# Kernel tuning notes

Measured on AMD Instinct MI355X. Metric: run time of the kernel, lower is better.

## Reference

```python
import jax, jax.numpy as jnp
import numpy as np

NU, NS, NV = 50000, 10000, 30000
D = 128
NUM_LAYERS = 2
EPS_US, EPS_UV, EPS_SV = 0.1, 0.1, 0.1
C_TEMP = 0.2
B = 2048


def _l2(x, eps=1e-12):
    n = jnp.sqrt(jnp.sum(x * x, axis=-1, keepdims=True))
    return x / jnp.maximum(n, eps)


def _spmm(row, col, val, x, n_out):
    # COO sparse @ dense: gather rows of x, scale, segment-reduce
    return jax.ops.segment_sum(val[:, None] * x[col], row, num_segments=n_out)


def _propagate(row, col, val, a, b, eps, key):
    feats = jnp.concatenate([a, b], axis=0)
    n = feats.shape[0]
    acc = feats  # layer-0 features are NOT normalized in the original
    for i in range(NUM_LAYERS):
        feats = _spmm(row, col, val, feats, n)
        noise = jax.random.uniform(jax.random.fold_in(key, i), feats.shape, feats.dtype)
        feats = feats + jnp.sign(feats) * _l2(noise) * eps
        acc = acc + _l2(feats)
    mean = acc / (NUM_LAYERS + 1)
    return mean[: a.shape[0]], mean[a.shape[0]:]


def _aggregate(row, col, val, x, n_out, eps, key):
    agg = _spmm(row, col, val, x, n_out)
    noise = jax.random.uniform(key, agg.shape, agg.dtype)
    return agg + jnp.sign(agg) * _l2(noise) * eps


def _mga(users_list, streamers_list, lin_w, lin_b):
    embs = [jnp.concatenate([u, s], axis=0) for u, s in zip(users_list, streamers_list)]
    query = jnp.stack(embs, axis=1)                      # (N, 3, D)
    key_e = jnp.broadcast_to(embs[0][:, None, :], query.shape)
    concat = jnp.concatenate([key_e, query], axis=2)     # (N, 3, 2D)
    logits = jnp.einsum('nkc,c->nk', concat, lin_w[0]) + lin_b[0]
    att = jax.nn.softmax(logits, axis=1)                 # (N, 3)
    out = jnp.einsum('nk,nkd->nd', att, query)
    return out[:NU], out[NU:]


def _c_loss(x):
    p = _l2(x[:, 0, :])
    pos = jnp.sum(p * p, axis=1) / C_TEMP
    ttl = jax.nn.logsumexp(p @ p.T / C_TEMP, axis=1)
    return -jnp.mean(pos - ttl)


def _forward(users_feature, streamers_feature, videos_feature, lin_w, lin_b,
             us_row, us_col, us_val, uv_row, uv_col, uv_val,
             sv_row, sv_col, sv_val,
             uv_agg_row, uv_agg_col, uv_agg_val,
             sv_agg_row, sv_agg_col, sv_agg_val, users, streamers):
    key = jax.random.key(42)
    k_us, k_uv, k_sv, k_auv, k_asv = jax.random.split(key, 5)
    US_u, US_s = _propagate(us_row, us_col, us_val, users_feature, streamers_feature, EPS_US, k_us)
    UV_u, UV_v = _propagate(uv_row, uv_col, uv_val, users_feature, videos_feature, EPS_UV, k_uv)
    UV_s = _aggregate(sv_agg_row, sv_agg_col, sv_agg_val, UV_v, NS, EPS_SV, k_asv)
    SV_s, SV_v = _propagate(sv_row, sv_col, sv_val, streamers_feature, videos_feature, EPS_SV, k_sv)
    SV_u = _aggregate(uv_agg_row, uv_agg_col, uv_agg_val, SV_v, NU, EPS_UV, k_auv)
    users_rep, streamers_rep = _mga([US_u, UV_u, SV_u], [US_s, UV_s, SV_s], lin_w, lin_b)
    s_emb = streamers_rep[streamers]                      # (B, K, D)
    u_emb = jnp.broadcast_to(users_rep[users], s_emb.shape)  # (B, K, D)
    pred = jnp.sum(u_emb * s_emb, axis=2)                 # (B, K)
    bpr = -jnp.mean(jax.nn.log_sigmoid(pred[:, :1] - pred[:, 1:]))
    c_loss = 0.5 * (_c_loss(u_emb) + _c_loss(s_emb))
    return bpr, c_loss


def setup_inputs() -> dict:
    rng = np.random.default_rng(0)

    def prop_graph(m, n, nnz):
        r = rng.integers(0, m, nnz)
        c = rng.integers(0, n, nnz)
        rows = np.concatenate([r, c + m])
        cols = np.concatenate([c + m, r])
        deg = np.bincount(rows, minlength=m + n).astype(np.float64)
        d = 1.0 / (np.sqrt(deg) + 1e-8)
        vals = (d[rows] * d[cols]).astype(np.float32)
        return rows.astype(np.int32), cols.astype(np.int32), vals, r, c

    def agg_graph(r, c, m):
        rowsum = np.bincount(r, minlength=m).astype(np.float64)
        vals = (1.0 / (rowsum + 1e-8))[r].astype(np.float32)
        return r.astype(np.int32), c.astype(np.int32), vals

    us_row, us_col, us_val, _, _ = prop_graph(NU, NS, 400000)
    uv_row, uv_col, uv_val, uv_r, uv_c = prop_graph(NU, NV, 600000)
    sv_row, sv_col, sv_val, sv_r, sv_c = prop_graph(NS, NV, 400000)
    uv_agg_row, uv_agg_col, uv_agg_val = agg_graph(uv_r, uv_c, NU)
    sv_agg_row, sv_agg_col, sv_agg_val = agg_graph(sv_r, sv_c, NS)

    key = jax.random.key(0)
    k1, k2, k3, k4, k6, k7 = jax.random.split(key, 6)
    xn = lambda k, m: jax.random.normal(k, (m, D), jnp.float32) * np.sqrt(2.0 / (m + D)).astype(np.float32)
    return {
        'users_feature': xn(k1, NU),
        'streamers_feature': xn(k2, NS),
        'videos_feature': xn(k3, NV),
        'lin_w': jax.random.uniform(k4, (1, 2 * D), jnp.float32, -1.0, 1.0) * np.sqrt(6.0 / (2 * D + 1)).astype(np.float32),
        'lin_b': jnp.zeros((1,), jnp.float32),
        'us_row': jnp.asarray(us_row), 'us_col': jnp.asarray(us_col), 'us_val': jnp.asarray(us_val),
        'uv_row': jnp.asarray(uv_row), 'uv_col': jnp.asarray(uv_col), 'uv_val': jnp.asarray(uv_val),
        'sv_row': jnp.asarray(sv_row), 'sv_col': jnp.asarray(sv_col), 'sv_val': jnp.asarray(sv_val),
        'uv_agg_row': jnp.asarray(uv_agg_row), 'uv_agg_col': jnp.asarray(uv_agg_col), 'uv_agg_val': jnp.asarray(uv_agg_val),
        'sv_agg_row': jnp.asarray(sv_agg_row), 'sv_agg_col': jnp.asarray(sv_agg_col), 'sv_agg_val': jnp.asarray(sv_agg_val),
        'users': jax.random.randint(k6, (B, 1), 0, NU, dtype=jnp.int32),
        'streamers': jax.random.randint(k7, (B, 2), 0, NS, dtype=jnp.int32),
    }


def reference(users_feature, streamers_feature, videos_feature, lin_w, lin_b,
              us_row, us_col, us_val, uv_row, uv_col, uv_val,
              sv_row, sv_col, sv_val,
              uv_agg_row, uv_agg_col, uv_agg_val,
              sv_agg_row, sv_agg_col, sv_agg_val, users, streamers):
    return _forward(users_feature, streamers_feature, videos_feature, lin_w, lin_b,
                    us_row, us_col, us_val, uv_row, uv_col, uv_val,
                    sv_row, sv_col, sv_val,
                    uv_agg_row, uv_agg_col, uv_agg_val,
                    sv_agg_row, sv_agg_col, sv_agg_val, users, streamers)
```

## Files before the change

### kernel.cpp

```cpp
#include <hip/hip_runtime.h>
#include <stdint.h>

#define D 128
constexpr int NUc = 50000, NSc = 10000, NVc = 30000, Bc = 2048;
constexpr int N_US = 60000, N_UV = 80000, N_SV = 40000, N_ALL = 90000;
constexpr int BW = 64;
constexpr int NBH = 1280;
constexpr int CHUNK = 4096;
constexpr int CAPE = 6144;

typedef _Float16 h2v __attribute__((ext_vector_type(2)));
typedef _Float16 h4v __attribute__((ext_vector_type(4)));

__host__ __device__ inline void threefry(uint32_t k0, uint32_t k1, uint32_t x0, uint32_t x1,
                                         uint32_t& o0, uint32_t& o1) {
  uint32_t ks2 = k0 ^ k1 ^ 0x1BD11BDAu;
  uint32_t v0 = x0 + k0, v1 = x1 + k1;
#define TFR(r) { v0 += v1; v1 = (v1 << (r)) | (v1 >> (32 - (r))); v1 ^= v0; }
  TFR(13) TFR(15) TFR(26) TFR(6)   v0 += k1;  v1 += ks2 + 1u;
  TFR(17) TFR(29) TFR(16) TFR(24)  v0 += ks2; v1 += k0 + 2u;
  TFR(13) TFR(15) TFR(26) TFR(6)   v0 += k0;  v1 += k1 + 3u;
  TFR(17) TFR(29) TFR(16) TFR(24)  v0 += k1;  v1 += ks2 + 4u;
  TFR(13) TFR(15) TFR(26) TFR(6)   v0 += ks2; v1 += k0 + 5u;
#undef TFR
  o0 = v0; o1 = v1;
}

__device__ __forceinline__ float unif01(uint32_t k0, uint32_t k1, uint32_t j) {
  uint32_t a, b;
  threefry(k0, k1, 0u, j, a, b);
  uint32_t bits = a ^ b;
  return __uint_as_float(0x3F800000u | (bits >> 9)) - 1.0f;
}

struct Bld {
  const int* rows[5]; const int* cols[5]; const float* vals[5];
  int* rp[5]; int* aux[5];
  int2* cv[5]; int2* ibuf[5];
  int* bhist;
  int eBase[6];
  int sBlkBase[6];
  int cBlkBase[6];
  int bktBase[6];
  int nPlus1[5];
};

__global__ void k_hist5(Bld b) {
  int gid = blockIdx.x * blockDim.x + threadIdx.x;
  if (gid >= b.eBase[5]) return;
  int g = 0;
  while (gid >= b.eBase[g + 1]) ++g;
  int e = gid - b.eBase[g];
  atomicAdd(&b.rp[g][b.rows[g][e] + 1], 1);
}

__global__ __launch_bounds__(1024) void k_scan1f(Bld b) {
  __shared__ int wsum[16];
  int blk = blockIdx.x;
  int g = 0;
  while (blk >= b.sBlkBase[g + 1]) ++g;
  int lb = blk - b.sBlkBase[g];
  int n = b.nPlus1[g];
  int* data = b.rp[g];
  int tid = threadIdx.x, lane = tid & 63, w = tid >> 6;
  int i = lb * 1024 + tid;
  int x = (i < n) ? data[i] : 0;
  for (int off = 1; off < 64; off <<= 1) {
    int t = __shfl_up(x, off, 64);
    if (lane >= off) x += t;
  }
  if (lane == 63) wsum[w] = x;
  __syncthreads();
  if (w == 0 && lane < 16) {
    int s = wsum[lane];
    for (int off = 1; off < 16; off <<= 1) {
      int t = __shfl_up(s, off, 64);
      if (lane >= off) s += t;
    }
    wsum[lane] = s;
  }
  __syncthreads();
  int woff = (w > 0) ? wsum[w - 1] : 0;
  if (i < n) data[i] = x + woff;
  if (tid == 1023) b.aux[g][lb] = x + woff;
}

__global__ void k_scan2f(Bld b) {
  int g = blockIdx.x;
  int nb = b.sBlkBase[g + 1] - b.sBlkBase[g];
  int* aux = b.aux[g];
  int lane = threadIdx.x;
  int carry = 0;
  for (int base = 0; base < nb; base += 64) {
    int i = base + lane;
    int v = (i < nb) ? aux[i] : 0;
    for (int off = 1; off < 64; off <<= 1) {
      int t = __shfl_up(v, off, 64);
      if (lane >= off) v += t;
    }
    if (i < nb) aux[i] = v + carry;
    carry += __shfl(v, 63, 64);
  }
}

__global__ __launch_bounds__(1024) void k_scan3f(Bld b) {
  int blk = blockIdx.x;
  int g = 0;
  while (blk >= b.sBlkBase[g + 1]) ++g;
  int lb = blk - b.sBlkBase[g];
  if (lb == 0) return;
  int i = lb * 1024 + threadIdx.x;
  if (i < b.nPlus1[g]) b.rp[g][i] += b.aux[g][lb - 1];
}

__global__ __launch_bounds__(256) void k_bhist(Bld b) {
  __shared__ int h[NBH];
  int blk = blockIdx.x;
  int g = 0;
  while (blk >= b.cBlkBase[g + 1]) ++g;
  int lblk = blk - b.cBlkBase[g];
  int nbkt = b.bktBase[g + 1] - b.bktBase[g];
  int tid = threadIdx.x;
  for (int i = tid; i < nbkt; i += 256) h[i] = 0;
  __syncthreads();
  int nnzg = b.eBase[g + 1] - b.eBase[g];
  int e0 = lblk * CHUNK;
  int eEnd = min(e0 + CHUNK, nnzg);
  for (int e = e0 + tid; e < eEnd; e += 256)
    atomicAdd(&h[b.rows[g][e] >> 6], 1);
  __syncthreads();
  int* outp = b.bhist + (size_t)blk * NBH;
  for (int i = tid; i < nbkt; i += 256) outp[i] = h[i];
}

__global__ void k_bscan(Bld b) {
  int gid = blockIdx.x * blockDim.x + threadIdx.x;
  int w = gid >> 6, lane = gid & 63;
  if (w >= b.bktBase[5]) return;
  int g = 0;
  while (w >= b.bktBase[g + 1]) ++g;
  int lb = w - b.bktBase[g];
  int carry = b.rp[g][lb * BW];
  int blk0 = b.cBlkBase[g], nblk = b.cBlkBase[g + 1] - blk0;
  for (int t = 0; t < nblk; t += 64) {
    int i = t + lane;
    int v = (i < nblk) ? b.bhist[(size_t)(blk0 + i) * NBH + lb] : 0;
    int x = v;
    for (int off = 1; off < 64; off <<= 1) {
      int tt = __shfl_up(x, off, 64);
      if (lane >= off) x += tt;
    }
    if (i < nblk) b.bhist[(size_t)(blk0 + i) * NBH + lb] = x - v + carry;
    carry += __shfl(x, 63, 64);
  }
}

__global__ __launch_bounds__(256) void k_bscat(Bld b) {
  __shared__ int cur[NBH];
  int blk = blockIdx.x;
  int g = 0;
  while (blk >= b.cBlkBase[g + 1]) ++g;
  int lblk = blk - b.cBlkBase[g];
  int nbkt = b.bktBase[g + 1] - b.bktBase[g];
  int tid = threadIdx.x;
  const int* bh = b.bhist + (size_t)blk * NBH;
  for (int i = tid; i < nbkt; i += 256) cur[i] = bh[i];
  __syncthreads();
  int nnzg = b.eBase[g + 1] - b.eBase[g];
  int e0 = lblk * CHUNK;
  int eEnd = min(e0 + CHUNK, nnzg);
  int2* ib = b.ibuf[g];
  for (int e = e0 + tid; e < eEnd; e += 256) {
    int row = b.rows[g][e];
    int pos = atomicAdd(&cur[row >> 6], 1);
    int packed = b.cols[g][e] | ((row & (BW - 1)) << 17);
    ib[pos] = make_int2(packed, __float_as_int(b.vals[g][e]));
  }
}

__global__ __launch_bounds__(256) void k_scatl2(Bld b) {
  __shared__ int lcur[BW];
  __shared__ int2 stg[CAPE];
  int bid = blockIdx.x;
  int g = 0;
  while (bid >= b.bktBase[g + 1]) ++g;
  int lb = bid - b.bktBase[g];
  int n = b.nPlus1[g] - 1;
  int r0 = lb * BW;
  int rowsInB = min(BW, n - r0);
  const int* rp = b.rp[g];
  int segStart = rp[r0];
  int segLen = rp[r0 + rowsInB] - segStart;
  int tid = threadIdx.x;
  if (tid < rowsInB) lcur[tid] = rp[r0 + tid] - segStart;
  __syncthreads();
  const int2* ib = b.ibuf[g];
  int2* cv = b.cv[g];
  for (int i = tid; i < segLen; i += 256) {
    int2 v = ib[segStart + i];
    int rowlow = ((uint32_t)v.x) >> 17;
    int2 outv = make_int2(v.x & 0x1FFFF, v.y);
    int lpos = atomicAdd(&lcur[rowlow], 1);
    if (lpos < CAPE) stg[lpos] = outv;
    else cv[segStart + lpos] = outv;
  }
  __syncthreads();
  int lim = min(segLen, CAPE);
  for (int i = tid; i < lim; i += 256) cv[segStart + i] = stg[i];
}

__global__ void k_l0(const float* __restrict__ u, const float* __restrict__ s,
                     const float* __restrict__ v, _Float16* __restrict__ L0) {
  int gid = blockIdx.x * blockDim.x + threadIdx.x;
  const int tot = N_ALL * (D / 4);
  if (gid >= tot) return;
  int r = gid >> 5, c4 = gid & 31;
  const float* src = (r < NUc) ? u + (size_t)r * D
                   : (r < NUc + NSc) ? s + (size_t)(r - NUc) * D
                                     : v + (size_t)(r - NUc - NSc) * D;
  float4 x = ((const float4*)src)[c4];
  ((h4v*)L0)[gid] = h4v{(_Float16)x.x, (_Float16)x.y, (_Float16)x.z, (_Float16)x.w};
}

__device__ __forceinline__ void gather_row(const int* __restrict__ rp,
                                           const int2* __restrict__ cv,
                                           const char* __restrict__ spc, int rl, uint32_t lo,
                                           int thr, int addLo, int addHi,
                                           float& fx, float& fy) {
  int s = rp[rl], e = rp[rl + 1];
  int k = s;
  for (; k + 3 < e; k += 4) {
    int2 q0 = cv[k], q1 = cv[k + 1], q2 = cv[k + 2], q3 = cv[k + 3];
    uint32_t c0 = (uint32_t)(q0.x + (q0.x >= thr ? addHi : addLo));
    uint32_t c1 = (uint32_t)(q1.x + (q1.x >= thr ? addHi : addLo));
    uint32_t c2 = (uint32_t)(q2.x + (q2.x >= thr ? addHi : addLo));
    uint32_t c3 = (uint32_t)(q3.x + (q3.x >= thr ? addHi : addLo));
    h2v x0 = *(const h2v*)(spc + (c0 << 8) + lo);
    h2v x1 = *(const h2v*)(spc + (c1 << 8) + lo);
    h2v x2 = *(const h2v*)(spc + (c2 << 8) + lo);
    h2v x3 = *(const h2v*)(spc + (c3 << 8) + lo);
    float v0 = __int_as_float(q0.y), v1 = __int_as_float(q1.y);
    float v2 = __int_as_float(q2.y), v3 = __int_as_float(q3.y);
    fx = fmaf(v0, (float)x0.x, fx); fy = fmaf(v0, (float)x0.y, fy);
    fx = fmaf(v1, (float)x1.x, fx); fy = fmaf(v1, (float)x1.y, fy);
    fx = fmaf(v2, (float)x2.x, fx); fy = fmaf(v2, (float)x2.y, fy);
    fx = fmaf(v3, (float)x3.x, fx); fy = fmaf(v3, (float)x3.y, fy);
  }
  for (; k < e; ++k) {
    int2 q = cv[k];
    uint32_t c = (uint32_t)(q.x + (q.x >= thr ? addHi : addLo));
    h2v x = *(const h2v*)(spc + (c << 8) + lo);
    float v = __int_as_float(q.y);
    fx = fmaf(v, (float)x.x, fx); fy = fmaf(v, (float)x.y, fy);
  }
}

struct GP {
  const int* rp[3]; const int2* cv[3];
  const _Float16* src[3];
  const _Float16* accIn[3];
  _Float16* accOut[3];
  _Float16* dst[3];
  uint32_t k0[3], k1[3];
  int thr[3], addLo[3], addHi[3];
  int rBase[4];
  float div;
};

__global__ void k_gprop3(GP p) {
  int gid = blockIdx.x * blockDim.x + threadIdx.x;
  int r = gid >> 6, lane = gid & 63;
  if (r >= p.rBase[3]) return;
  int g = 0;
  while (r >= p.rBase[g + 1]) ++g;
  int rl = r - p.rBase[g];
  uint32_t lo = (uint32_t)lane << 2;
  float fx = 0.f, fy = 0.f;
  gather_row(p.rp[g], p.cv[g], (const char*)p.src[g], rl, lo,
             p.thr[g], p.addLo[g], p.addHi[g], fx, fy);
  uint32_t j0 = (uint32_t)rl * D + (uint32_t)lane * 2;
  float u0 = unif01(p.k0[g], p.k1[g], j0);
  float u1 = unif01(p.k0[g], p.k1[g], j0 + 1u);
  float s2 = u0 * u0 + u1 * u1;
  for (int m = 1; m < 64; m <<= 1) s2 += __shfl_xor(s2, m, 64);
  float nn = fmaxf(sqrtf(s2), 1e-12f);
  float sg0 = (fx > 0.f) ? 1.f : ((fx < 0.f) ? -1.f : 0.f);
  float sg1 = (fy > 0.f) ? 1.f : ((fy < 0.f) ? -1.f : 0.f);
  float nf0 = fx + sg0 * (u0 / nn) * 0.1f;
  float nf1 = fy + sg1 * (u1 / nn) * 0.1f;
  float fs = nf0 * nf0 + nf1 * nf1;
  for (int m = 1; m < 64; m <<= 1) fs += __shfl_xor(fs, m, 64);
  float fn = fmaxf(sqrtf(fs), 1e-12f);
  int gr = rl + (rl >= p.thr[g] ? p.addHi[g] : p.addLo[g]);
  h2v ai = ((const h2v*)p.accIn[g])[(size_t)gr * (D / 2) + lane];
  float ax = ((float)ai.x + nf0 / fn) / p.div;
  float ay = ((float)ai.y + nf1 / fn) / p.div;
  ((h2v*)p.accOut[g])[(size_t)rl * (D / 2) + lane] = h2v{(_Float16)ax, (_Float16)ay};
  if (p.dst[g])
    ((h2v*)p.dst[g])[(size_t)rl * (D / 2) + lane] = h2v{(_Float16)nf0, (_Float16)nf1};
}

struct GA {
  const int* rp[2]; const int2* cv[2];
  const _Float16* src[2]; _Float16* dst[2];
  uint32_t k0[2], k1[2];
  int rBase[3];
};

__global__ void k_gagg2(GA a) {
  int gid = blockIdx.x * blockDim.x + threadIdx.x;
  int r = gid >> 6, lane = gid & 63;
  if (r >= a.rBase[2]) return;
  int g = (r >= a.rBase[1]) ? 1 : 0;
  int rl = r - a.rBase[g];
  uint32_t lo = (uint32_t)lane << 2;
  float fx = 0.f, fy = 0.f;
  gather_row(a.rp[g], a.cv[g], (const char*)a.src[g], rl, lo, 0x7fffffff, 0, 0, fx, fy);
  uint32_t j0 = (uint32_t)rl * D + (uint32_t)lane * 2;
  float u0 = unif01(a.k0[g], a.k1[g], j0);
  float u1 = unif01(a.k0[g], a.k1[g], j0 + 1u);
  float s2 = u0 * u0 + u1 * u1;
  for (int m = 1; m < 64; m <<= 1) s2 += __shfl_xor(s2, m, 64);
  float nn = fmaxf(sqrtf(s2), 1e-12f);
  float sg0 = (fx > 0.f) ? 1.f : ((fx < 0.f) ? -1.f : 0.f);
  float sg1 = (fy > 0.f) ? 1.f : ((fy < 0.f) ? -1.f : 0.f);
  ((h2v*)a.dst[g])[(size_t)rl * (D / 2) + lane] =
      h2v{(_Float16)(fx + sg0 * (u0 / nn) * 0.1f), (_Float16)(fy + sg1 * (u1 / nn) * 0.1f)};
}

__global__ void k_mga(_Float16* __restrict__ e0buf, const _Float16* __restrict__ UVa,
                      const _Float16* __restrict__ UVs, const _Float16* __restrict__ SVu,
                      const _Float16* __restrict__ SVa, const float* __restrict__ w,
                      const float* __restrict__ bptr) {
  int gid = blockIdx.x * blockDim.x + threadIdx.x;
  int wave = gid >> 6, lane = gid & 63;
  int n = NUc + NSc;
  if (wave >= n) return;
  const _Float16* e1 = (wave < NUc) ? UVa + (size_t)wave * D : UVs + (size_t)(wave - NUc) * D;
  const _Float16* e2 = (wave < NUc) ? SVu + (size_t)wave * D : SVa + (size_t)(wave - NUc) * D;
  _Float16* e0 = e0buf + (size_t)wave * D;
  int c = lane * 2;
  h2v h0 = *(const h2v*)(e0 + c), h1 = *(const h2v*)(e1 + c), h2_ = *(const h2v*)(e2 + c);
  float2 v0 = {(float)h0.x, (float)h0.y};
  float2 v1 = {(float)h1.x, (float)h1.y};
  float2 v2 = {(float)h2_.x, (float)h2_.y};
  float2 wl = *(const float2*)(w + c);
  float2 wh = *(const float2*)(w + D + c);
  float d00 = v0.x * wl.x + v0.y * wl.y;
  float c0 = v0.x * wh.x + v0.y * wh.y;
  float c1 = v1.x * wh.x + v1.y * wh.y;
  float c2 = v2.x * wh.x + v2.y * wh.y;
  for (int m = 1; m < 64; m <<= 1) {
    d00 += __shfl_xor(d00, m, 64);
    c0 += __shfl_xor(c0, m, 64);
    c1 += __shfl_xor(c1, m, 64);
    c2 += __shfl_xor(c2, m, 64);
  }
  float b = bptr[0];
  float l0 = d00 + c0 + b, l1 = d00 + c1 + b, l2v = d00 + c2 + b;
  float mx = fmaxf(l0, fmaxf(l1, l2v));
  float a0 = expf(l0 - mx), a1 = expf(l1 - mx), a2 = expf(l2v - mx);
  float s = a0 + a1 + a2;
  a0 /= s; a1 /= s; a2 /= s;
  float ox = a0 * v0.x + a1 * v1.x + a2 * v2.x;
  float oy = a0 * v0.y + a1 * v1.y + a2 * v2.y;
  *(h2v*)(e0 + c) = h2v{(_Float16)ox, (_Float16)oy};
}

__global__ void k_batch(const _Float16* __restrict__ reps, const int* __restrict__ users,
                        const int* __restrict__ streamers, float* __restrict__ Pu,
                        float* __restrict__ Ps, float* __restrict__ accs) {
  int gid = blockIdx.x * blockDim.x + threadIdx.x;
  int wave = gid >> 6, lane = gid & 63;
  if (wave >= Bc) return;
  int u = users[wave];
  int s0 = streamers[wave * 2], s1 = streamers[wave * 2 + 1];
  h2v uh = ((const h2v*)(reps + (size_t)u * D))[lane];
  h2v ah = ((const h2v*)(reps + (size_t)(NUc + s0) * D))[lane];
  h2v ch = ((const h2v*)(reps + (size_t)(NUc + s1) * D))[lane];
  float2 uv = {(float)uh.x, (float)uh.y};
  float2 av = {(float)ah.x, (float)ah.y};
  float2 cv = {(float)ch.x, (float)ch.y};
  float p0 = uv.x * av.x + uv.y * av.y;
  float p1 = uv.x * cv.x + uv.y * cv.y;
  float un = uv.x * uv.x + uv.y * uv.y;
  float an = av.x * av.x + av.y * av.y;
  for (int m = 1; m < 64; m <<= 1) {
    p0 += __shfl_xor(p0, m, 64);
    p1 += __shfl_xor(p1, m, 64);
    un += __shfl_xor(un, m, 64);
    an += __shfl_xor(an, m, 64);
  }
  if (lane == 0) {
    float t = p0 - p1;
    float term = fmaxf(-t, 0.f) + log1pf(expf(-fabsf(t)));
    atomicAdd(&accs[0], term);
  }
  float und = fmaxf(sqrtf(un), 1e-12f);
  float andv = fmaxf(sqrtf(an), 1e-12f);
  ((float2*)(Pu + (size_t)wave * D))[lane] = float2{uv.x / und, uv.y / und};
  ((float2*)(Ps + (size_t)wave * D))[lane] = float2{av.x / andv, av.y / andv};
}

__global__ __launch_bounds__(256) void k_cgemm(const float* __restrict__ Pu,
                                               const float* __restrict__ Ps,
                                               float* __restrict__ Su,
                                               float* __restrict__ Ss) {
  const float* P = blockIdx.z ? Ps : Pu;
  float* S = blockIdx.z ? Ss : Su;
  __shared__ float A[32][132];
  __shared__ float BT[128][68];
  int tid = threadIdx.x;
  int tx = tid & 15, ty = tid >> 4;
  int brow0 = blockIdx.x * 32;
  int j0 = blockIdx.y * 512;
#pragma unroll
  for (int i = 0; i < 4; ++i) {
    int idx = tid + i * 256;
    int r = idx >> 5, c4 = idx & 31;
    float4 v = ((const float4*)(P + (size_t)(brow0 + r) * D))[c4];
    *(float4*)&A[r][c4 * 4] = v;
  }
  float s[2] = {0.f, 0.f};
  for (int jt = 0; jt < 8; ++jt) {
    __syncthreads();
#pragma unroll
    for (int i = 0; i < 8; ++i) {
      int idx = tid + i * 256;
      int r = idx >> 5, c4 = idx & 31;
      float4 v = ((const float4*)(P + (size_t)(j0 + jt * 64 + r) * D))[c4];
      BT[c4 * 4 + 0][r] = v.x;
      BT[c4 * 4 + 1][r] = v.y;
      BT[c4 * 4 + 2][r] = v.z;
      BT[c4 * 4 + 3][r] = v.w;
    }
    __syncthreads();
    float acc[2][4] = {};
    for (int k = 0; k < 128; k += 4) {
      float4 a0 = *(const float4*)&A[ty * 2 + 0][k];
      float4 a1 = *(const float4*)&A[ty * 2 + 1][k];
      float4 b0 = *(const float4*)&BT[k + 0][tx * 4];
      float4 b1 = *(const float4*)&BT[k + 1][tx * 4];
      float4 b2 = *(const float4*)&BT[k + 2][tx * 4];
      float4 b3 = *(const float4*)&BT[k + 3][tx * 4];
      acc[0][0] = fmaf(a0.x, b0.x, acc[0][0]); acc[0][1] = fmaf(a0.x, b0.y, acc[0][1]);
      acc[0][2] = fmaf(a0.x, b0.z, acc[0][2]); acc[0][3] = fmaf(a0.x, b0.w, acc[0][3]);
      acc[1][0] = fmaf(a1.x, b0.x, acc[1][0]); acc[1][1] = fmaf(a1.x, b0.y, acc[1][1]);
      acc[1][2] = fmaf(a1.x, b0.z, acc[1][2]); acc[1][3] = fmaf(a1.x, b0.w, acc[1][3]);
      acc[0][0] = fmaf(a0.y, b1.x, acc[0][0]); acc[0][1] = fmaf(a0.y, b1.y, acc[0][1]);
      acc[0][2] = fmaf(a0.y, b1.z, acc[0][2]); acc[0][3] = fmaf(a0.y, b1.w, acc[0][3]);
      acc[1][0] = fmaf(a1.y, b1.x, acc[1][0]); acc[1][1] = fmaf(a1.y, b1.y, acc[1][1]);
      acc[1][2] = fmaf(a1.y, b1.z, acc[1][2]); acc[1][3] = fmaf(a1.y, b1.w, acc[1][3]);
      acc[0][0] = fmaf(a0.z, b2.x, acc[0][0]); acc[0][1] = fmaf(a0.z, b2.y, acc[0][1]);
      acc[0][2] = fmaf(a0.z, b2.z, acc[0][2]); acc[0][3] = fmaf(a0.z, b2.w, acc[0][3]);
      acc[1][0] = fmaf(a1.z, b2.x, acc[1][0]); acc[1][1] = fmaf(a1.z, b2.y, acc[1][1]);
      acc[1][2] = fmaf(a1.z, b2.z, acc[1][2]); acc[1][3] = fmaf(a1.z, b2.w, acc[1][3]);
      acc[0][0] = fmaf(a0.w, b3.x, acc[0][0]); acc[0][1] = fmaf(a0.w, b3.y, acc[0][1]);
      acc[0][2] = fmaf(a0.w, b3.z, acc[0][2]); acc[0][3] = fmaf(a0.w, b3.w, acc[0][3]);
      acc[1][0] = fmaf(a1.w, b3.x, acc[1][0]); acc[1][1] = fmaf(a1.w, b3.y, acc[1][1]);
      acc[1][2] = fmaf(a1.w, b3.z, acc[1][2]); acc[1][3] = fmaf(a1.w, b3.w, acc[1][3]);
    }
#pragma unroll
    for (int i = 0; i < 2; ++i)
#pragma unroll
      for (int jj = 0; jj < 4; ++jj) s[i] += __expf(5.0f * acc[i][jj]);
  }
#pragma unroll
  for (int i = 0; i < 2; ++i) {
    for (int off = 1; off < 16; off <<= 1) s[i] += __shfl_xor(s[i], off, 64);
    if (tx == 0) atomicAdd(&S[brow0 + ty * 2 + i], s[i]);
  }
}

__global__ void k_cfinal(const float* __restrict__ Pu, const float* __restrict__ Ps,
                         const float* __restrict__ Su, const float* __restrict__ Ss,
                         float* __restrict__ accs) {
  int gid = blockIdx.x * blockDim.x + threadIdx.x;
  int wave = gid >> 6, lane = gid & 63;
  if (wave >= 2 * Bc) return;
  int loss = wave >> 11, b = wave & (Bc - 1);
  const float* P = loss ? Ps : Pu;
  const float* S = loss ? Ss : Su;
  float2 p = ((const float2*)(P + (size_t)b * D))[lane];
  float pos = p.x * p.x + p.y * p.y;
  for (int m = 1; m < 64; m <<= 1) pos += __shfl_xor(pos, m, 64);
  if (lane == 0) atomicAdd(&accs[1 + loss], logf(S[b]) - 5.0f * pos);
}

__global__ void k_final(const float* __restrict__ accs, float* __restrict__ out) {
  if (threadIdx.x == 0 && blockIdx.x == 0) {
    out[0] = accs[0] / (float)Bc;
    out[1] = 0.5f * (accs[1] + accs[2]) / (float)Bc;
  }
}

extern "C" void kernel_launch(void* const* d_in, const int* in_sizes, int n_in,
                              void* d_out, int out_size, void* d_ws, size_t ws_size,
                              hipStream_t stream) {
  const float* usersF = (const float*)d_in[0];
  const float* streamersF = (const float*)d_in[1];
  const float* videosF = (const float*)d_in[2];
  const float* linW = (const float*)d_in[3];
  const float* linB = (const float*)d_in[4];
  const int* grows[5] = {(const int*)d_in[5], (const int*)d_in[8], (const int*)d_in[11],
                         (const int*)d_in[14], (const int*)d_in[17]};
  const int* gcols[5] = {(const int*)d_in[6], (const int*)d_in[9], (const int*)d_in[12],
                         (const int*)d_in[15], (const int*)d_in[18]};
  const float* gvals[5] = {(const float*)d_in[7], (const float*)d_in[10], (const float*)d_in[13],
                           (const float*)d_in[16], (const float*)d_in[19]};
  const int* users = (const int*)d_in[20];
  const int* streamers = (const int*)d_in[21];
  int nnz[5] = {in_sizes[5], in_sizes[8], in_sizes[11], in_sizes[14], in_sizes[17]};
  int gn[5] = {N_US, N_UV, N_SV, NUc, NSc};
  float* out = (float*)d_out;

  char* pb = (char*)d_ws;
  auto allocH = [&](size_t nh) { _Float16* p = (_Float16*)pb; pb += nh * 2; return p; };
  _Float16* L0 = allocH((size_t)N_ALL * D);
  _Float16* Th[3] = {allocH((size_t)N_US * D), allocH((size_t)N_UV * D), allocH((size_t)N_SV * D)};
  _Float16* Ac[3] = {allocH((size_t)N_US * D), allocH((size_t)N_UV * D), allocH((size_t)N_SV * D)};
  _Float16* UVsH = allocH((size_t)NSc * D);
  _Float16* SVuH = allocH((size_t)NUc * D);
  pb = (char*)(((uintptr_t)pb + 15) & ~(uintptr_t)15);
  float* Pu = (float*)pb; pb += (size_t)Bc * D * 4;
  float* Ps = (float*)pb; pb += (size_t)Bc * D * 4;
  float* accs = (float*)pb; pb += 16 * 4;
  float* Su = (float*)pb; pb += Bc * 4;
  float* Ss = (float*)pb; pb += Bc * 4;
  int totE = nnz[0] + nnz[1] + nnz[2] + nnz[3] + nnz[4];
  int2* cvAll = (int2*)pb; pb += (size_t)totE * 8;
  int2* ibAll = (int2*)pb; pb += (size_t)totE * 8;
  int* rpAll = (int*)pb;
  int totRP = 0;
  for (int g = 0; g < 5; ++g) totRP += gn[g] + 1;
  pb += (size_t)totRP * 4;
  int* auxAll = (int*)pb; pb += 5 * 128 * 4;

  Bld b;
  int totCBlk = 0;
  {
    int eA = 0, sA = 0, rpO = 0, cvO = 0, bA = 0, cA = 0;
    for (int g = 0; g < 5; ++g) {
      b.rows[g] = grows[g]; b.cols[g] = gcols[g]; b.vals[g] = gvals[g];
      b.eBase[g] = eA; eA += nnz[g];
      int n1 = gn[g] + 1;
      b.nPlus1[g] = n1;
      b.sBlkBase[g] = sA; sA += (n1 + 1023) / 1024;
      b.cBlkBase[g] = cA; cA += (nnz[g] + CHUNK - 1) / CHUNK;
      b.rp[g] = rpAll + rpO; rpO += n1;
      b.aux[g] = auxAll + g * 128;
      b.cv[g] = cvAll + cvO;
      b.ibuf[g] = ibAll + cvO; cvO += nnz[g];
      b.bktBase[g] = bA; bA += (gn[g] + BW - 1) / BW;
    }
    b.eBase[5] = eA;
    b.sBlkBase[5] = sA;
    b.cBlkBase[5] = cA;
    b.bktBase[5] = bA;
    totCBlk = cA;
  }
  int totBlk = b.sBlkBase[5];
  int totBkt = b.bktBase[5];
  int* bhistAll = (int*)pb; pb += (size_t)totCBlk * NBH * 4;
  b.bhist = bhistAll;

  uint32_t kus[2], kuv[2], ksv[2], kauv[2], kasv[2];
  threefry(0u, 42u, 0u, 0u, kus[0], kus[1]);
  threefry(0u, 42u, 0u, 1u, kuv[0], kuv[1]);
  threefry(0u, 42u, 0u, 2u, ksv[0], ksv[1]);
  threefry(0u, 42u, 0u, 3u, kauv[0], kauv[1]);
  threefry(0u, 42u, 0u, 4u, kasv[0], kasv[1]);
  uint32_t kusL[2][2], kuvL[2][2], ksvL[2][2];
  for (uint32_t i = 0; i < 2; ++i) {
    threefry(kus[0], kus[1], 0u, i, kusL[i][0], kusL[i][1]);
    threefry(kuv[0], kuv[1], 0u, i, kuvL[i][0], kuvL[i][1]);
    threefry(ksv[0], ksv[1], 0u, i, ksvL[i][0], ksvL[i][1]);
  }

  hipMemsetAsync(rpAll, 0, (size_t)totRP * sizeof(int), stream);
  k_hist5<<<(unsigned)((totE + 255) / 256), 256, 0, stream>>>(b);
  k_scan1f<<<(unsigned)totBlk, 1024, 0, stream>>>(b);
  k_scan2f<<<5, 64, 0, stream>>>(b);
  k_scan3f<<<(unsigned)totBlk, 1024, 0, stream>>>(b);
  k_bhist<<<(unsigned)totCBlk, 256, 0, stream>>>(b);
  k_bscan<<<(unsigned)(((size_t)totBkt * 64 + 255) / 256), 256, 0, stream>>>(b);
  k_bscat<<<(unsigned)totCBlk, 256, 0, stream>>>(b);
  k_scatl2<<<(unsigned)totBkt, 256, 0, stream>>>(b);

  k_l0<<<(unsigned)((N_ALL * (D / 4) + 255) / 256), 256, 0, stream>>>(usersF, streamersF,
                                                                      videosF, L0);

  GP p1, p2;
  const uint32_t* kL1[3] = {kusL[0], kuvL[0], ksvL[0]};
  const uint32_t* kL2[3] = {kusL[1], kuvL[1], ksvL[1]};
  int rB[4] = {0, N_US, N_US + N_UV, N_US + N_UV + N_SV};
  int thr1[3] = {0x7fffffff, NUc, 0};
  int aLo1[3] = {0, 0, NUc};
  int aHi1[3] = {0, NSc, NUc};
  for (int g = 0; g < 3; ++g) {
    p1.rp[g] = b.rp[g]; p1.cv[g] = b.cv[g];
    p1.src[g] = L0; p1.accIn[g] = L0; p1.accOut[g] = Ac[g]; p1.dst[g] = Th[g];
    p1.k0[g] = kL1[g][0]; p1.k1[g] = kL1[g][1];
    p1.thr[g] = thr1[g]; p1.addLo[g] = aLo1[g]; p1.addHi[g] = aHi1[g];
    p1.rBase[g] = rB[g];
    p2.rp[g] = b.rp[g]; p2.cv[g] = b.cv[g];
    p2.src[g] = Th[g]; p2.accIn[g] = Ac[g]; p2.accOut[g] = Ac[g]; p2.dst[g] = nullptr;
    p2.k0[g] = kL2[g][0]; p2.k1[g] = kL2[g][1];
    p2.thr[g] = 0x7fffffff; p2.addLo[g] = 0; p2.addHi[g] = 0;
    p2.rBase[g] = rB[g];
  }
  p1.rBase[3] = rB[3]; p2.rBase[3] = rB[3];
  p1.div = 1.0f; p2.div = 3.0f;
  unsigned gpropBlocks = (unsigned)(((size_t)rB[3] * 64 + 255) / 256);
  k_gprop3<<<gpropBlocks, 256, 0, stream>>>(p1);
  k_gprop3<<<gpropBlocks, 256, 0, stream>>>(p2);

  GA ga;
  ga.rp[0] = b.rp[3]; ga.cv[0] = b.cv[3];
  ga.src[0] = Ac[2] + (size_t)NSc * D;
  ga.dst[0] = SVuH; ga.k0[0] = kauv[0]; ga.k1[0] = kauv[1];
  ga.rp[1] = b.rp[4]; ga.cv[1] = b.cv[4];
  ga.src[1] = Ac[1] + (size_t)NUc * D;
  ga.dst[1] = UVsH; ga.k0[1] = kasv[0]; ga.k1[1] = kasv[1];
  ga.rBase[0] = 0; ga.rBase[1] = NUc; ga.rBase[2] = NUc + NSc;
  k_gagg2<<<(unsigned)(((size_t)(NUc + NSc) * 64 + 255) / 256), 256, 0, stream>>>(ga);

  k_mga<<<(unsigned)((NUc + NSc + 3) / 4), 256, 0, stream>>>(Ac[0], Ac[1], UVsH, SVuH, Ac[2],
                                                             linW, linB);
  hipMemsetAsync(accs, 0, (size_t)(16 + 2 * Bc) * sizeof(float), stream);
  k_batch<<<(unsigned)((Bc + 3) / 4), 256, 0, stream>>>(Ac[0], users, streamers, Pu, Ps, accs);
  k_cgemm<<<dim3(Bc / 32, 4, 2), 256, 0, stream>>>(Pu, Ps, Su, Ss);
  k_cfinal<<<(unsigned)((2 * Bc + 3) / 4), 256, 0, stream>>>(Pu, Ps, Su, Ss, accs);
  k_final<<<1, 64, 0, stream>>>(accs, out);
}
```

Measured before the change: 919.2 us.

## Pre-remap columns and use packed fp16 multiply-accumulate in SpMM gathers

The column-index remap into the concatenated feature table now happens once while the CSR is built, and edge values are stored as duplicated fp16 pairs. The inner gather loop can then do packed half2 multiply-adds into four fp16 accumulators, with no per-edge compare or fp32 converts. Layer-1 outputs are written at global row offsets so that layer 2 gathers without remapping. Accumulating in fp16 lowers precision and may lose accuracy on high-degree rows.

```diff
diff --git a/kernel.cpp b/kernel.cpp
--- a/kernel.cpp
+++ b/kernel.cpp
@@ -43,6 +43,7 @@
   int cBlkBase[6];
   int bktBase[6];
   int nPlus1[5];
+  int thrC[5], addC[5];
 };
 
 __global__ void k_hist5(Bld b) {
@@ -170,11 +171,15 @@
   int e0 = lblk * CHUNK;
   int eEnd = min(e0 + CHUNK, nnzg);
   int2* ib = b.ibuf[g];
+  int thr = b.thrC[g], add = b.addC[g];
   for (int e = e0 + tid; e < eEnd; e += 256) {
     int row = b.rows[g][e];
+    int c = b.cols[g][e];
+    c += (c >= thr) ? add : 0;
+    float v = b.vals[g][e];
+    uint32_t hb = (uint32_t)__builtin_bit_cast(unsigned short, (_Float16)v);
     int pos = atomicAdd(&cur[row >> 6], 1);
-    int packed = b.cols[g][e] | ((row & (BW - 1)) << 17);
-    ib[pos] = make_int2(packed, __float_as_int(b.vals[g][e]));
+    ib[pos] = make_int2(c | ((row & (BW - 1)) << 17), (int)(hb | (hb << 16)));
   }
 }
 
@@ -225,44 +230,38 @@
 __device__ __forceinline__ void gather_row(const int* __restrict__ rp,
                                            const int2* __restrict__ cv,
                                            const char* __restrict__ spc, int rl, uint32_t lo,
-                                           int thr, int addLo, int addHi,
                                            float& fx, float& fy) {
   int s = rp[rl], e = rp[rl + 1];
+  h2v a0 = {0, 0}, a1 = {0, 0}, a2 = {0, 0}, a3 = {0, 0};
   int k = s;
   for (; k + 3 < e; k += 4) {
     int2 q0 = cv[k], q1 = cv[k + 1], q2 = cv[k + 2], q3 = cv[k + 3];
-    uint32_t c0 = (uint32_t)(q0.x + (q0.x >= thr ? addHi : addLo));
-    uint32_t c1 = (uint32_t)(q1.x + (q1.x >= thr ? addHi : addLo));
-    uint32_t c2 = (uint32_t)(q2.x + (q2.x >= thr ? addHi : addLo));
-    uint32_t c3 = (uint32_t)(q3.x + (q3.x >= thr ? addHi : addLo));
-    h2v x0 = *(const h2v*)(spc + (c0 << 8) + lo);
-    h2v x1 = *(const h2v*)(spc + (c1 << 8) + lo);
-    h2v x2 = *(const h2v*)(spc + (c2 << 8) + lo);
-    h2v x3 = *(const h2v*)(spc + (c3 << 8) + lo);
-    float v0 = __int_as_float(q0.y), v1 = __int_as_float(q1.y);
-    float v2 = __int_as_float(q2.y), v3 = __int_as_float(q3.y);
-    fx = fmaf(v0, (float)x0.x, fx); fy = fmaf(v0, (float)x0.y, fy);
-    fx = fmaf(v1, (float)x1.x, fx); fy = fmaf(v1, (float)x1.y, fy);
-    fx = fmaf(v2, (float)x2.x, fx); fy = fmaf(v2, (float)x2.y, fy);
-    fx = fmaf(v3, (float)x3.x, fx); fy = fmaf(v3, (float)x3.y, fy);
+    h2v x0 = *(const h2v*)(spc + ((uint32_t)q0.x << 8) + lo);
+    h2v x1 = *(const h2v*)(spc + ((uint32_t)q1.x << 8) + lo);
+    h2v x2 = *(const h2v*)(spc + ((uint32_t)q2.x << 8) + lo);
+    h2v x3 = *(const h2v*)(spc + ((uint32_t)q3.x << 8) + lo);
+    a0 += x0 * __builtin_bit_cast(h2v, q0.y);
+    a1 += x1 * __builtin_bit_cast(h2v, q1.y);
+    a2 += x2 * __builtin_bit_cast(h2v, q2.y);
+    a3 += x3 * __builtin_bit_cast(h2v, q3.y);
   }
   for (; k < e; ++k) {
     int2 q = cv[k];
-    uint32_t c = (uint32_t)(q.x + (q.x >= thr ? addHi : addLo));
-    h2v x = *(const h2v*)(spc + (c << 8) + lo);
-    float v = __int_as_float(q.y);
-    fx = fmaf(v, (float)x.x, fx); fy = fmaf(v, (float)x.y, fy);
-  }
+    h2v x = *(const h2v*)(spc + ((uint32_t)q.x << 8) + lo);
+    a0 += x * __builtin_bit_cast(h2v, q.y);
+  }
+  fx = (float)a0.x + (float)a1.x + (float)a2.x + (float)a3.x;
+  fy = (float)a0.y + (float)a1.y + (float)a2.y + (float)a3.y;
 }
 
 struct GP {
   const int* rp[3]; const int2* cv[3];
-  const _Float16* src[3];
+  const char* src[3];
   const _Float16* accIn[3];
   _Float16* accOut[3];
   _Float16* dst[3];
   uint32_t k0[3], k1[3];
-  int thr[3], addLo[3], addHi[3];
+  int rowThr[3], rowAdd[3];
   int rBase[4];
   float div;
 };
@@ -275,9 +274,8 @@
   while (r >= p.rBase[g + 1]) ++g;
   int rl = r - p.rBase[g];
   uint32_t lo = (uint32_t)lane << 2;
-  float fx = 0.f, fy = 0.f;
-  gather_row(p.rp[g], p.cv[g], (const char*)p.src[g], rl, lo,
-             p.thr[g], p.addLo[g], p.addHi[g], fx, fy);
+  float fx, fy;
+  gather_row(p.rp[g], p.cv[g], p.src[g], rl, lo, fx, fy);
   uint32_t j0 = (uint32_t)rl * D + (uint32_t)lane * 2;
   float u0 = unif01(p.k0[g], p.k1[g], j0);
   float u1 = unif01(p.k0[g], p.k1[g], j0 + 1u);
@@ -291,18 +289,18 @@
   float fs = nf0 * nf0 + nf1 * nf1;
   for (int m = 1; m < 64; m <<= 1) fs += __shfl_xor(fs, m, 64);
   float fn = fmaxf(sqrtf(fs), 1e-12f);
-  int gr = rl + (rl >= p.thr[g] ? p.addHi[g] : p.addLo[g]);
+  int gr = rl + ((rl >= p.rowThr[g]) ? p.rowAdd[g] : 0);
   h2v ai = ((const h2v*)p.accIn[g])[(size_t)gr * (D / 2) + lane];
   float ax = ((float)ai.x + nf0 / fn) / p.div;
   float ay = ((float)ai.y + nf1 / fn) / p.div;
   ((h2v*)p.accOut[g])[(size_t)rl * (D / 2) + lane] = h2v{(_Float16)ax, (_Float16)ay};
   if (p.dst[g])
-    ((h2v*)p.dst[g])[(size_t)rl * (D / 2) + lane] = h2v{(_Float16)nf0, (_Float16)nf1};
+    ((h2v*)p.dst[g])[(size_t)gr * (D / 2) + lane] = h2v{(_Float16)nf0, (_Float16)nf1};
 }
 
 struct GA {
   const int* rp[2]; const int2* cv[2];
-  const _Float16* src[2]; _Float16* dst[2];
+  const char* src[2]; _Float16* dst[2];
   uint32_t k0[2], k1[2];
   int rBase[3];
 };
@@ -314,8 +312,8 @@
   int g = (r >= a.rBase[1]) ? 1 : 0;
   int rl = r - a.rBase[g];
   uint32_t lo = (uint32_t)lane << 2;
-  float fx = 0.f, fy = 0.f;
-  gather_row(a.rp[g], a.cv[g], (const char*)a.src[g], rl, lo, 0x7fffffff, 0, 0, fx, fy);
+  float fx, fy;
+  gather_row(a.rp[g], a.cv[g], a.src[g], rl, lo, fx, fy);
   uint32_t j0 = (uint32_t)rl * D + (uint32_t)lane * 2;
   float u0 = unif01(a.k0[g], a.k1[g], j0);
   float u1 = unif01(a.k0[g], a.k1[g], j0 + 1u);
@@ -517,7 +515,9 @@
   char* pb = (char*)d_ws;
   auto allocH = [&](size_t nh) { _Float16* p = (_Float16*)pb; pb += nh * 2; return p; };
   _Float16* L0 = allocH((size_t)N_ALL * D);
-  _Float16* Th[3] = {allocH((size_t)N_US * D), allocH((size_t)N_UV * D), allocH((size_t)N_SV * D)};
+  _Float16* Th0 = allocH((size_t)N_US * D);
+  _Float16* Th1 = allocH((size_t)N_ALL * D);
+  _Float16* Th2 = allocH((size_t)N_SV * D);
   _Float16* Ac[3] = {allocH((size_t)N_US * D), allocH((size_t)N_UV * D), allocH((size_t)N_SV * D)};
   _Float16* UVsH = allocH((size_t)NSc * D);
   _Float16* SVuH = allocH((size_t)NUc * D);
@@ -540,8 +540,11 @@
   int totCBlk = 0;
   {
     int eA = 0, sA = 0, rpO = 0, cvO = 0, bA = 0, cA = 0;
+    int thrC[5] = {0x7fffffff, NUc, 0, 0x7fffffff, 0x7fffffff};
+    int addC[5] = {0, NSc, NUc, 0, 0};
     for (int g = 0; g < 5; ++g) {
       b.rows[g] = grows[g]; b.cols[g] = gcols[g]; b.vals[g] = gvals[g];
+      b.thrC[g] = thrC[g]; b.addC[g] = addC[g];
       b.eBase[g] = eA; eA += nnz[g];
       int n1 = gn[g] + 1;
       b.nPlus1[g] = n1;
@@ -594,19 +597,21 @@
   const uint32_t* kL1[3] = {kusL[0], kuvL[0], ksvL[0]};
   const uint32_t* kL2[3] = {kusL[1], kuvL[1], ksvL[1]};
   int rB[4] = {0, N_US, N_US + N_UV, N_US + N_UV + N_SV};
-  int thr1[3] = {0x7fffffff, NUc, 0};
-  int aLo1[3] = {0, 0, NUc};
-  int aHi1[3] = {0, NSc, NUc};
+  int rThr[3] = {0x7fffffff, NUc, 0};
+  int rAdd[3] = {0, NSc, NUc};
+  _Float16* dstP[3] = {Th0, Th1, Th2 - (size_t)NUc * D};
+  const char* src2[3] = {(const char*)Th0, (const char*)Th1,
+                         (const char*)Th2 - (size_t)NUc * D * 2};
   for (int g = 0; g < 3; ++g) {
     p1.rp[g] = b.rp[g]; p1.cv[g] = b.cv[g];
-    p1.src[g] = L0; p1.accIn[g] = L0; p1.accOut[g] = Ac[g]; p1.dst[g] = Th[g];
+    p1.src[g] = (const char*)L0; p1.accIn[g] = L0; p1.accOut[g] = Ac[g]; p1.dst[g] = dstP[g];
     p1.k0[g] = kL1[g][0]; p1.k1[g] = kL1[g][1];
-    p1.thr[g] = thr1[g]; p1.addLo[g] = aLo1[g]; p1.addHi[g] = aHi1[g];
+    p1.rowThr[g] = rThr[g]; p1.rowAdd[g] = rAdd[g];
     p1.rBase[g] = rB[g];
     p2.rp[g] = b.rp[g]; p2.cv[g] = b.cv[g];
-    p2.src[g] = Th[g]; p2.accIn[g] = Ac[g]; p2.accOut[g] = Ac[g]; p2.dst[g] = nullptr;
+    p2.src[g] = src2[g]; p2.accIn[g] = Ac[g]; p2.accOut[g] = Ac[g]; p2.dst[g] = nullptr;
     p2.k0[g] = kL2[g][0]; p2.k1[g] = kL2[g][1];
-    p2.thr[g] = 0x7fffffff; p2.addLo[g] = 0; p2.addHi[g] = 0;
+    p2.rowThr[g] = 0x7fffffff; p2.rowAdd[g] = 0;
     p2.rBase[g] = rB[g];
   }
   p1.rBase[3] = rB[3]; p2.rBase[3] = rB[3];
@@ -617,10 +622,10 @@
 
   GA ga;
   ga.rp[0] = b.rp[3]; ga.cv[0] = b.cv[3];
-  ga.src[0] = Ac[2] + (size_t)NSc * D;
+  ga.src[0] = (const char*)(Ac[2] + (size_t)NSc * D);
   ga.dst[0] = SVuH; ga.k0[0] = kauv[0]; ga.k1[0] = kauv[1];
   ga.rp[1] = b.rp[4]; ga.cv[1] = b.cv[4];
-  ga.src[1] = Ac[1] + (size_t)NUc * D;
+  ga.src[1] = (const char*)(Ac[1] + (size_t)NUc * D);
   ga.dst[1] = UVsH; ga.k0[1] = kasv[0]; ga.k1[1] = kasv[1];
   ga.rBase[0] = 0; ga.rBase[1] = NUc; ga.rBase[2] = NUc + NSc;
   k_gagg2<<<(unsigned)(((size_t)(NUc + NSc) * 64 + 255) / 256), 256, 0, stream>>>(ga);
```

New measurement: 920.6 us. About the same (+0.1%).
